# Optimization experiments

Hardware: AMD Instinct MI355X
Metric: run time of the kernel (lower is better)

The kernel has to match this reference:

```python
import jax, jax.numpy as jnp
import numpy as np

NEG_SLOPE = 0.2  # PyG GATConv default LeakyReLU slope


def add_self_loops(edge_index, n):
    loops = jnp.arange(n, dtype=edge_index.dtype)
    return jnp.concatenate([edge_index, jnp.stack([loops, loops])], axis=1)


def segment_softmax(e, seg, n):
    # e: [E, H], seg: [E] destination node ids
    m = jax.ops.segment_max(e, seg, num_segments=n)          # [N, H]
    ex = jnp.exp(e - m[seg])
    s = jax.ops.segment_sum(ex, seg, num_segments=n)          # [N, H]
    return ex / (s[seg] + 1e-16)


def gat_conv(x, edge_index, W, att_src, att_dst, bias, heads, concat):
    n = x.shape[0]
    c = W.shape[1] // heads
    ei = add_self_loops(edge_index, n)
    src, dst = ei[0], ei[1]
    h = (x @ W).reshape(n, heads, c)                          # [N, H, C]
    a_src = jnp.einsum('nhc,hc->nh', h, att_src)              # [N, H]
    a_dst = jnp.einsum('nhc,hc->nh', h, att_dst)
    e = a_src[src] + a_dst[dst]                               # [E, H]
    e = jax.nn.leaky_relu(e, NEG_SLOPE)
    alpha = segment_softmax(e, dst, n)                        # [E, H]
    msg = alpha[:, :, None] * h[src]                          # [E, H, C]
    out = jax.ops.segment_sum(msg, dst, num_segments=n)       # [N, H, C]
    if concat:
        out = out.reshape(n, heads * c)
    else:
        out = out.mean(axis=1)
    return out + bias


def setup_inputs() -> dict:
    key = jax.random.key(0)
    ks = jax.random.split(key, 16)
    N, E, IN, HID, H, OUT = 50000, 1600000, 512, 256, 8, 128
    s = 0.1
    return {
        'x': jax.random.normal(ks[0], (N, IN), jnp.float32),
        'edge_index': jax.random.randint(ks[1], (2, E), 0, N, jnp.int64),
        'edge_index_2': jax.random.randint(ks[2], (2, E), 0, N, jnp.int64),
        'W1': jax.random.normal(ks[3], (IN, HID * H), jnp.float32) * s,
        'att_src1': jax.random.normal(ks[4], (H, HID), jnp.float32) * s,
        'att_dst1': jax.random.normal(ks[5], (H, HID), jnp.float32) * s,
        'b1': jnp.zeros((HID * H,), jnp.float32),
        'W2': jax.random.normal(ks[6], (HID * H, OUT), jnp.float32) * s,
        'att_src2': jax.random.normal(ks[7], (1, OUT), jnp.float32) * s,
        'att_dst2': jax.random.normal(ks[8], (1, OUT), jnp.float32) * s,
        'b2': jnp.zeros((OUT,), jnp.float32),
        'W3': jax.random.normal(ks[9], (HID * H, OUT), jnp.float32) * s,
        'att_src3': jax.random.normal(ks[10], (1, OUT), jnp.float32) * s,
        'att_dst3': jax.random.normal(ks[11], (1, OUT), jnp.float32) * s,
        'b3': jnp.zeros((OUT,), jnp.float32),
    }


def reference(x, edge_index, edge_index_2, W1, att_src1, att_dst1, b1,
              W2, att_src2, att_dst2, b2, W3, att_src3, att_dst3, b3):
    # Inference mode: F.dropout and GATConv attention dropout are no-ops.
    emb = jax.nn.elu(gat_conv(x, edge_index, W1, att_src1, att_dst1, b1, heads=8, concat=True))
    x1 = gat_conv(emb, edge_index, W2, att_src2, att_dst2, b2, heads=1, concat=False)
    x2 = gat_conv(emb, edge_index_2, W3, att_src3, att_dst3, b3, heads=1, concat=False)
    logits = jax.nn.softmax(x1, axis=1)    # nn.Softmax() legacy dim -> 1 for 2D
    logits_2 = jax.nn.softmax(x2, axis=1)
    predictions = jnp.argmax(logits, axis=1)
    return (logits, logits_2, predictions)
```

## Files before the change

### kernel.cpp

```cpp
#include <hip/hip_runtime.h>
#include <hip/hip_bf16.h>
#include <math.h>

#define N_NODES 50000
#define E_EDGES 1600000
#define EP_EDGES (E_EDGES + N_NODES)
#define IN_F 512
#define HID 256
#define HEADS 8
#define OUTF 128

typedef unsigned short u16;
typedef __attribute__((ext_vector_type(8))) short short8;
typedef __attribute__((ext_vector_type(4))) float floatx4;

static __device__ __forceinline__ float eluf(float x) {
  return x > 0.f ? x : expm1f(x);
}

static __device__ __forceinline__ u16 bf16_hi(float v) {
  __hip_bfloat16 h = __float2bfloat16(v);
  return *(u16*)&h;
}
static __device__ __forceinline__ float bf16_f(u16 u) {
  __hip_bfloat16 h = *(__hip_bfloat16*)&u;
  return __bfloat162float(h);
}
static __device__ __forceinline__ void split3_bf16(float v, u16& h, u16& m, u16& l) {
  h = bf16_hi(v);
  float r1 = v - bf16_f(h);
  m = bf16_hi(r1);
  float r2 = r1 - bf16_f(m);
  l = bf16_hi(r2);
}

static __device__ __forceinline__ int clampi(int v, int n) {
  return v < 0 ? 0 : (v >= n ? n - 1 : v);
}


__global__ void k_detect(const int* __restrict__ ei, int* __restrict__ flag) {
  __shared__ int nz;
  if (threadIdx.x == 0) nz = 0;
  __syncthreads();
  for (int i = threadIdx.x; i < 4096; i += blockDim.x)
    if (ei[2 * i + 1] != 0) nz = 1;
  __syncthreads();
  if (threadIdx.x == 0) *flag = (nz ? 0 : 1);
}

__global__ void k_init_deg(int* __restrict__ deg, int n) {
  int i = blockIdx.x * 256 + threadIdx.x;
  if (i < n) deg[i] = 1;
}

__global__ void k_count(const int* __restrict__ ei, const int* __restrict__ flag,
                        int* __restrict__ deg, int E) {
  int e = blockIdx.x * 256 + threadIdx.x;
  if (e >= E) return;
  int f = *flag;
  int idx = E + e;
  int dst = clampi(ei[f ? 2 * idx : idx], N_NODES);
  atomicAdd(&deg[dst], 1);
}

__global__ __launch_bounds__(1024) void k_scan(const int* __restrict__ deg,
                                               int* __restrict__ rp, int n) {
  __shared__ int sw[16];
  __shared__ int s_run;
  int tid = threadIdx.x, lane = tid & 63, w = tid >> 6;
  if (tid == 0) s_run = 0;
  __syncthreads();
  for (int base = 0; base < n; base += 1024) {
    int i = base + tid;
    int v = (i < n) ? deg[i] : 0;
    int sv = v;
#pragma unroll
    for (int off = 1; off < 64; off <<= 1) {
      int t = __shfl_up(sv, off);
      if (lane >= off) sv += t;
    }
    if (lane == 63) sw[w] = sv;
    __syncthreads();
    if (w == 0) {
      int wsum = (lane < 16) ? sw[lane] : 0;
#pragma unroll
      for (int off = 1; off < 16; off <<= 1) {
        int t = __shfl_up(wsum, off);
        if (lane >= off) wsum += t;
      }
      if (lane < 16) sw[lane] = wsum;
    }
    __syncthreads();
    int woff = (w > 0) ? sw[w - 1] : 0;
    int run = s_run;
    if (i < n) rp[i + 1] = run + woff + sv;
    __syncthreads();
    if (tid == 1023) s_run = run + sw[15];
    __syncthreads();
  }
  if (tid == 0) rp[0] = 0;
}

__global__ void k_fill_self(const int* __restrict__ rp, int* __restrict__ wp,
                            int* __restrict__ col, int n) {
  int i = blockIdx.x * 256 + threadIdx.x;
  if (i < n) { int p = rp[i]; col[p] = i; wp[i] = p + 1; }
}

__global__ void k_fill_edges(const int* __restrict__ ei, const int* __restrict__ flag,
                             int* __restrict__ wp, int* __restrict__ col, int E) {
  int e = blockIdx.x * 256 + threadIdx.x;
  if (e >= E) return;
  int f = *flag;
  int src = clampi(ei[f ? 2 * e : e], N_NODES);
  int didx = E + e;
  int dst = clampi(ei[f ? 2 * didx : didx], N_NODES);
  int p = atomicAdd(&wp[dst], 1);
  col[p] = src;
}

__global__ void k_split3_t(const float* __restrict__ W, u16* __restrict__ H,
                           u16* __restrict__ Mv, u16* __restrict__ L,
                           int kshift, int kmask, int Nw, int total) {
  int idx = blockIdx.x * 256 + threadIdx.x;
  if (idx >= total) return;
  int n = idx >> kshift;
  int k = idx & kmask;
  u16 h, m, l;
  split3_bf16(W[(size_t)k * Nw + n], h, m, l);
  H[idx] = h;
  Mv[idx] = m;
  L[idx] = l;
}

__global__ __launch_bounds__(256) void k_watt1(
    const float* __restrict__ W1, const float* __restrict__ attS,
    const float* __restrict__ attD, float* __restrict__ watt) {
  int wid = (blockIdx.x * 256 + threadIdx.x) >> 6;
  int lane = threadIdx.x & 63;
  if (wid >= IN_F * HEADS) return;
  int k = wid >> 3, h = wid & 7;
  float4 wv = *(const float4*)&W1[(size_t)k * (HID * HEADS) + h * HID + lane * 4];
  float4 sv = *(const float4*)&attS[h * HID + lane * 4];
  float4 dv = *(const float4*)&attD[h * HID + lane * 4];
  float s = wv.x * sv.x + wv.y * sv.y + wv.z * sv.z + wv.w * sv.w;
  float d = wv.x * dv.x + wv.y * dv.y + wv.z * dv.z + wv.w * dv.w;
  for (int off = 32; off; off >>= 1) {
    s += __shfl_xor(s, off);
    d += __shfl_xor(d, off);
  }
  if (lane == 0) {
    watt[(size_t)(2 * h) * IN_F + k] = s;
    watt[(size_t)(2 * h + 1) * IN_F + k] = d;
  }
}

__global__ __launch_bounds__(256) void k_asad1(
    const float* __restrict__ x, const float* __restrict__ watt,
    float* __restrict__ asall, float* __restrict__ adall, int n) {
  int node = (blockIdx.x * 256 + threadIdx.x) >> 6;
  int lane = threadIdx.x & 63;
  if (node >= n) return;
  float4 x0 = *(const float4*)&x[(size_t)node * IN_F + lane * 8];
  float4 x1 = *(const float4*)&x[(size_t)node * IN_F + lane * 8 + 4];
  for (int h = 0; h < HEADS; ++h) {
    const float* ws = watt + (size_t)(2 * h) * IN_F + lane * 8;
    const float* wd = watt + (size_t)(2 * h + 1) * IN_F + lane * 8;
    float4 s0 = *(const float4*)ws, s1 = *(const float4*)(ws + 4);
    float4 d0 = *(const float4*)wd, d1 = *(const float4*)(wd + 4);
    float s = x0.x * s0.x + x0.y * s0.y + x0.z * s0.z + x0.w * s0.w
            + x1.x * s1.x + x1.y * s1.y + x1.z * s1.z + x1.w * s1.w;
    float d = x0.x * d0.x + x0.y * d0.y + x0.z * d0.z + x0.w * d0.w
            + x1.x * d1.x + x1.y * d1.y + x1.z * d1.z + x1.w * d1.w;
    for (int off = 32; off; off >>= 1) {
      s += __shfl_xor(s, off);
      d += __shfl_xor(d, off);
    }
    if (lane == 0) {
      asall[(size_t)h * n + node] = s;
      adall[(size_t)h * n + node] = d;
    }
  }
}

#define GBM 128
#define GBN 128
#define GBK 32
#define GM1 391

#define MFMA_BF16 __builtin_amdgcn_mfma_f32_16x16x32_bf16

__device__ __forceinline__ void gemm_epilogue(floatx4 acc[4][4], float* C,
                                              int ldc, int M, int accum,
                                              int row0, int col0, int wr,
                                              int wc, int lane) {
  int q = lane >> 4, n15 = lane & 15;
#pragma unroll
  for (int i = 0; i < 4; ++i) {
#pragma unroll
    for (int r = 0; r < 4; ++r) {
      int row = row0 + wr * 64 + i * 16 + q * 4 + r;
      if (row < M) {
#pragma unroll
        for (int j = 0; j < 4; ++j) {
          int cg = col0 + wc * 64 + j * 16 + n15;
          float v = acc[i][j][r];
          if (accum) v += C[(size_t)row * ldc + cg];
          C[(size_t)row * ldc + cg] = v;
        }
      }
    }
  }
}

__device__ __forceinline__ void gemm1_core(
    const float* __restrict__ X, int lda,
    const u16* __restrict__ Bh, const u16* __restrict__ Bm,
    const u16* __restrict__ Bl, int ldb,
    float* __restrict__ C, int ldc, int M, int K, int row0, int col0,
    u16* lds) {
  int tid = threadIdx.x;
  int lane = tid & 63, wave = tid >> 6;
  int wr = wave >> 1, wc = wave & 1;
  floatx4 acc[4][4] = {};
  int m0 = tid >> 2, m1 = (tid + 256) >> 2;
  int q0 = tid & 3;
  int lo0 = ((m0 >> 4) * 64 + q0 * 16 + (m0 & 15)) * 8;
  int lo1 = ((m1 >> 4) * 64 + q0 * 16 + (m1 & 15)) * 8;

  for (int k0 = 0; k0 < K; k0 += GBK) {
#pragma unroll
    for (int c = 0; c < 2; ++c) {
      int m = c ? m1 : m0;
      int lo = c ? lo1 : lo0;
      int gr = row0 + m;
      float f[8];
      if (gr < M) {
        float4 f0 = *(const float4*)(X + (size_t)gr * lda + k0 + q0 * 8);
        float4 f1 = *(const float4*)(X + (size_t)gr * lda + k0 + q0 * 8 + 4);
        f[0] = f0.x; f[1] = f0.y; f[2] = f0.z; f[3] = f0.w;
        f[4] = f1.x; f[5] = f1.y; f[6] = f1.z; f[7] = f1.w;
      } else {
#pragma unroll
        for (int e = 0; e < 8; ++e) f[e] = 0.f;
      }
      short8 vh, vm, vl;
#pragma unroll
      for (int e = 0; e < 8; ++e) {
        u16 h, m2, l;
        split3_bf16(f[e], h, m2, l);
        vh[e] = (short)h; vm[e] = (short)m2; vl[e] = (short)l;
      }
      *(short8*)&lds[lo] = vh;
      *(short8*)&lds[4096 + lo] = vm;
      *(short8*)&lds[8192 + lo] = vl;
    }
#pragma unroll
    for (int c = 0; c < 2; ++c) {
      int m = c ? m1 : m0;
      int lo = c ? lo1 : lo0;
      size_t go = (size_t)(col0 + m) * ldb + k0 + q0 * 8;
      *(short8*)&lds[12288 + lo] = *(const short8*)(Bh + go);
      *(short8*)&lds[16384 + lo] = *(const short8*)(Bm + go);
      *(short8*)&lds[20480 + lo] = *(const short8*)(Bl + go);
    }
    __syncthreads();
    short8 a_h[4], a_m[4], a_l[4];
#pragma unroll
    for (int i = 0; i < 4; ++i) {
      int o = ((wr * 4 + i) * 64 + lane) * 8;
      a_h[i] = *(short8*)&lds[o];
      a_m[i] = *(short8*)&lds[4096 + o];
      a_l[i] = *(short8*)&lds[8192 + o];
    }
#pragma unroll
    for (int j = 0; j < 4; ++j) {
      int o = ((wc * 4 + j) * 64 + lane) * 8;
      short8 b_h = *(short8*)&lds[12288 + o];
      short8 b_m = *(short8*)&lds[16384 + o];
      short8 b_l = *(short8*)&lds[20480 + o];
#pragma unroll
      for (int i = 0; i < 4; ++i) {
        acc[i][j] = MFMA_BF16(a_l[i], b_h, acc[i][j], 0, 0, 0);
        acc[i][j] = MFMA_BF16(a_m[i], b_m, acc[i][j], 0, 0, 0);
        acc[i][j] = MFMA_BF16(a_h[i], b_l, acc[i][j], 0, 0, 0);
        acc[i][j] = MFMA_BF16(a_m[i], b_h, acc[i][j], 0, 0, 0);
        acc[i][j] = MFMA_BF16(a_h[i], b_m, acc[i][j], 0, 0, 0);
        acc[i][j] = MFMA_BF16(a_h[i], b_h, acc[i][j], 0, 0, 0);
      }
    }
    __syncthreads();
  }
  gemm_epilogue(acc, C, ldc, M, 0, row0, col0, wr, wc, lane);
}

__global__ __launch_bounds__(256) void gemm1_k(
    const float* __restrict__ X, int lda,
    const u16* __restrict__ Bh, const u16* __restrict__ Bm,
    const u16* __restrict__ Bl, int ldb,
    float* __restrict__ C, int ldc, int M, int K) {
  __shared__ __align__(16) u16 lds[24576];
  gemm1_core(X, lda, Bh, Bm, Bl, ldb, C, ldc, M, K,
             blockIdx.x * GBM, blockIdx.y * GBN, lds);
}

__device__ __forceinline__ void gemm_core6(
    const u16* __restrict__ Ah, const u16* __restrict__ Am,
    const u16* __restrict__ Al, int lda,
    const u16* __restrict__ Bh, const u16* __restrict__ Bm,
    const u16* __restrict__ Bl, int ldb,
    float* __restrict__ C, int ldc, int M, int K, int row0, int col0,
    int accum, u16* lds) {
  int tid = threadIdx.x;
  int lane = tid & 63, wave = tid >> 6;
  int wr = wave >> 1, wc = wave & 1;
  floatx4 acc[4][4] = {};
  int m0 = tid >> 2, m1 = (tid + 256) >> 2;
  int q0 = tid & 3;
  int lo0 = ((m0 >> 4) * 64 + q0 * 16 + (m0 & 15)) * 8;
  int lo1 = ((m1 >> 4) * 64 + q0 * 16 + (m1 & 15)) * 8;
  for (int k0 = 0; k0 < K; k0 += GBK) {
#pragma unroll
    for (int c = 0; c < 2; ++c) {
      int m = c ? m1 : m0;
      int lo = c ? lo1 : lo0;
      int gr = row0 + m;
      short8 vh = {}, vm = {}, vl = {};
      if (gr < M) {
        size_t go = (size_t)gr * lda + k0 + q0 * 8;
        vh = *(const short8*)(Ah + go);
        vm = *(const short8*)(Am + go);
        vl = *(const short8*)(Al + go);
      }
      *(short8*)&lds[lo] = vh;
      *(short8*)&lds[4096 + lo] = vm;
      *(short8*)&lds[8192 + lo] = vl;
      size_t go = (size_t)(col0 + m) * ldb + k0 + q0 * 8;
      *(short8*)&lds[12288 + lo] = *(const short8*)(Bh + go);
      *(short8*)&lds[16384 + lo] = *(const short8*)(Bm + go);
      *(short8*)&lds[20480 + lo] = *(const short8*)(Bl + go);
    }
    __syncthreads();
    short8 a_h[4], a_m[4], a_l[4];
#pragma unroll
    for (int i = 0; i < 4; ++i) {
      int o = ((wr * 4 + i) * 64 + lane) * 8;
      a_h[i] = *(short8*)&lds[o];
      a_m[i] = *(short8*)&lds[4096 + o];
      a_l[i] = *(short8*)&lds[8192 + o];
    }
#pragma unroll
    for (int j = 0; j < 4; ++j) {
      int o = ((wc * 4 + j) * 64 + lane) * 8;
      short8 b_h = *(short8*)&lds[12288 + o];
      short8 b_m = *(short8*)&lds[16384 + o];
      short8 b_l = *(short8*)&lds[20480 + o];
#pragma unroll
      for (int i = 0; i < 4; ++i) {
        acc[i][j] = MFMA_BF16(a_l[i], b_h, acc[i][j], 0, 0, 0);
        acc[i][j] = MFMA_BF16(a_m[i], b_m, acc[i][j], 0, 0, 0);
        acc[i][j] = MFMA_BF16(a_h[i], b_l, acc[i][j], 0, 0, 0);
        acc[i][j] = MFMA_BF16(a_m[i], b_h, acc[i][j], 0, 0, 0);
        acc[i][j] = MFMA_BF16(a_h[i], b_m, acc[i][j], 0, 0, 0);
        acc[i][j] = MFMA_BF16(a_h[i], b_h, acc[i][j], 0, 0, 0);
      }
    }
    __syncthreads();
  }
  gemm_epilogue(acc, C, ldc, M, accum, row0, col0, wr, wc, lane);
}

__device__ __forceinline__ void gemm_core3(
    const u16* __restrict__ Ah, const u16* __restrict__ Am, int lda,
    const u16* __restrict__ Bh, const u16* __restrict__ Bm, int ldb,
    float* __restrict__ C, int ldc, int M, int K, int row0, int col0,
    int accum, u16* lds) {
  int tid = threadIdx.x;
  int lane = tid & 63, wave = tid >> 6;
  int wr = wave >> 1, wc = wave & 1;
  floatx4 acc[4][4] = {};
  int m0 = tid >> 2, m1 = (tid + 256) >> 2;
  int q0 = tid & 3;
  int lo0 = ((m0 >> 4) * 64 + q0 * 16 + (m0 & 15)) * 8;
  int lo1 = ((m1 >> 4) * 64 + q0 * 16 + (m1 & 15)) * 8;
  for (int k0 = 0; k0 < K; k0 += GBK) {
#pragma unroll
    for (int c = 0; c < 2; ++c) {
      int m = c ? m1 : m0;
      int lo = c ? lo1 : lo0;
      int gr = row0 + m;
      short8 vh = {}, vm = {};
      if (gr < M) {
        size_t go = (size_t)gr * lda + k0 + q0 * 8;
        vh = *(const short8*)(Ah + go);
        vm = *(const short8*)(Am + go);
      }
      *(short8*)&lds[lo] = vh;
      *(short8*)&lds[4096 + lo] = vm;
      size_t go = (size_t)(col0 + m) * ldb + k0 + q0 * 8;
      *(short8*)&lds[12288 + lo] = *(const short8*)(Bh + go);
      *(short8*)&lds[16384 + lo] = *(const short8*)(Bm + go);
    }
    __syncthreads();
    short8 a_h[4], a_m[4];
#pragma unroll
    for (int i = 0; i < 4; ++i) {
      int o = ((wr * 4 + i) * 64 + lane) * 8;
      a_h[i] = *(short8*)&lds[o];
      a_m[i] = *(short8*)&lds[4096 + o];
    }
#pragma unroll
    for (int j = 0; j < 4; ++j) {
      int o = ((wc * 4 + j) * 64 + lane) * 8;
      short8 b_h = *(short8*)&lds[12288 + o];
      short8 b_m = *(short8*)&lds[16384 + o];
#pragma unroll
      for (int i = 0; i < 4; ++i) {
        acc[i][j] = MFMA_BF16(a_m[i], b_h, acc[i][j], 0, 0, 0);
        acc[i][j] = MFMA_BF16(a_h[i], b_m, acc[i][j], 0, 0, 0);
        acc[i][j] = MFMA_BF16(a_h[i], b_h, acc[i][j], 0, 0, 0);
      }
    }
    __syncthreads();
  }
  gemm_epilogue(acc, C, ldc, M, accum, row0, col0, wr, wc, lane);
}

__global__ __launch_bounds__(256) void gemm23_k(
    const u16* __restrict__ Ah, const u16* __restrict__ Am,
    const u16* __restrict__ Al, int lda,
    const u16* __restrict__ B2h, const u16* __restrict__ B2m,
    const u16* __restrict__ B2l,
    const u16* __restrict__ B3h, const u16* __restrict__ B3m, int ldb,
    float* __restrict__ C2, float* __restrict__ C3, int ldc, int M, int K,
    int accum) {
  __shared__ __align__(16) u16 lds[24576];
  if (blockIdx.z == 0)
    gemm_core6(Ah, Am, Al, lda, B2h, B2m, B2l, ldb, C2, ldc, M, K,
               blockIdx.x * GBM, 0, accum, lds);
  else
    gemm_core3(Ah, Am, lda, B3h, B3m, ldb, C3, ldc, M, K,
               blockIdx.x * GBM, 0, accum, lds);
}

template <int C>
__global__ __launch_bounds__(256) void att_dot(
    const float* __restrict__ h, const float* __restrict__ attS,
    const float* __restrict__ attD, float* __restrict__ aS,
    float* __restrict__ aD, int n) {
  int node = (blockIdx.x * 256 + threadIdx.x) >> 6;
  int lane = threadIdx.x & 63;
  if (node >= n) return;
  float s = 0.f, d = 0.f;
  if (C == 256) {
    float4 hv = *(const float4*)&h[(size_t)node * C + lane * 4];
    float4 sv = *(const float4*)&attS[lane * 4];
    float4 dv = *(const float4*)&attD[lane * 4];
    s = hv.x * sv.x + hv.y * sv.y + hv.z * sv.z + hv.w * sv.w;
    d = hv.x * dv.x + hv.y * dv.y + hv.z * dv.z + hv.w * dv.w;
  } else {
    float2 hv = *(const float2*)&h[(size_t)node * C + lane * 2];
    float2 sv = *(const float2*)&attS[lane * 2];
    float2 dv = *(const float2*)&attD[lane * 2];
    s = hv.x * sv.x + hv.y * sv.y;
    d = hv.x * dv.x + hv.y * dv.y;
  }
  for (int off = 32; off; off >>= 1) {
    s += __shfl_xor(s, off);
    d += __shfl_xor(d, off);
  }
  if (lane == 0) { aS[node] = s; aD[node] = d; }
}

static __device__ __forceinline__ void aggr_l1_core(
    int node, int lane,
    const int* __restrict__ rp, const int* __restrict__ col,
    const float* __restrict__ aS, const float* __restrict__ aD,
    const float* __restrict__ h, const float* __restrict__ bias,
    u16* __restrict__ embH, u16* __restrict__ embM, u16* __restrict__ embL,
    int ecol0, int ldE, int n) {
  int s0 = rp[node], s1 = rp[node + 1];
  int d = s1 - s0;
  float ad = aD[node];
  float4 acc = make_float4(0.f, 0.f, 0.f, 0.f);

  if (d <= 64) {
    int c = 0;
    float e = -3.0e38f;
    if (lane < d) {
      c = clampi(col[s0 + lane], n);
      float t = aS[c] + ad;
      e = t >= 0.f ? t : 0.2f * t;
    }
    float m = e;
    for (int off = 32; off; off >>= 1) m = fmaxf(m, __shfl_xor(m, off));
    float ex = (lane < d) ? expf(e - m) : 0.f;
    float s = ex;
    for (int off = 32; off; off >>= 1) s += __shfl_xor(s, off);
    float al = ex * (1.f / (s + 1e-16f));
    int dd = d & ~15;
    for (int j = 0; j < dd; j += 16) {
#pragma unroll
      for (int t = 0; t < 16; ++t) {
        int ct = __shfl(c, j + t);
        float at = __shfl(al, j + t);
        float4 hv = *(const float4*)&h[(size_t)ct * HID + lane * 4];
        acc.x += at * hv.x; acc.y += at * hv.y;
        acc.z += at * hv.z; acc.w += at * hv.w;
      }
    }
    if (dd < d) {
#pragma unroll
      for (int t = 0; t < 16; ++t) {
        if (dd + t < d) {
          int ct = __shfl(c, dd + t);
          float at = __shfl(al, dd + t);
          float4 hv = *(const float4*)&h[(size_t)ct * HID + lane * 4];
          acc.x += at * hv.x; acc.y += at * hv.y;
          acc.z += at * hv.z; acc.w += at * hv.w;
        }
      }
    }
  } else {
    float m = -3.0e38f;
    for (int i = s0 + lane; i < s1; i += 64) {
      float e = aS[clampi(col[i], n)] + ad;
      e = e >= 0.f ? e : 0.2f * e;
      m = fmaxf(m, e);
    }
    for (int off = 32; off; off >>= 1) m = fmaxf(m, __shfl_xor(m, off));
    float sum = 0.f;
    for (int i = s0 + lane; i < s1; i += 64) {
      float e = aS[clampi(col[i], n)] + ad;
      e = e >= 0.f ? e : 0.2f * e;
      sum += expf(e - m);
    }
    for (int off = 32; off; off >>= 1) sum += __shfl_xor(sum, off);
    float inv = 1.f / (sum + 1e-16f);
    for (int i = s0; i < s1; ++i) {
      int ci = clampi(col[i], n);
      float e = aS[ci] + ad;
      e = e >= 0.f ? e : 0.2f * e;
      float a = expf(e - m) * inv;
      float4 hv = *(const float4*)&h[(size_t)ci * HID + lane * 4];
      acc.x += a * hv.x; acc.y += a * hv.y; acc.z += a * hv.z; acc.w += a * hv.w;
    }
  }

  float4 bb = *(const float4*)&bias[lane * 4];
  float v0 = eluf(acc.x + bb.x);
  float v1 = eluf(acc.y + bb.y);
  float v2 = eluf(acc.z + bb.z);
  float v3 = eluf(acc.w + bb.w);
  ushort4 uh, um, ul;
  split3_bf16(v0, uh.x, um.x, ul.x);
  split3_bf16(v1, uh.y, um.y, ul.y);
  split3_bf16(v2, uh.z, um.z, ul.z);
  split3_bf16(v3, uh.w, um.w, ul.w);
  size_t o = (size_t)node * ldE + ecol0 + lane * 4;
  *(ushort4*)&embH[o] = uh;
  *(ushort4*)&embM[o] = um;
  *(ushort4*)&embL[o] = ul;
}

__global__ __launch_bounds__(256) void aggr_l1_fused(
    const int* __restrict__ rp, const int* __restrict__ col,
    const float* __restrict__ aS, const float* __restrict__ aD,
    const float* __restrict__ h, const float* __restrict__ bias,
    u16* __restrict__ embH, u16* __restrict__ embM, u16* __restrict__ embL,
    int ecol0, int ldE, int n) {
  int node = (blockIdx.x * 256 + threadIdx.x) >> 6;
  int lane = threadIdx.x & 63;
  if (node >= n) return;
  aggr_l1_core(node, lane, rp, col, aS, aD, h, bias, embH, embM, embL,
               ecol0, ldE, n);
}

__global__ __launch_bounds__(256) void fused_step(
    const int* __restrict__ rp, const int* __restrict__ col,
    const float* __restrict__ aS, const float* __restrict__ aD,
    const float* __restrict__ hg, const float* __restrict__ bias,
    u16* __restrict__ embH, u16* __restrict__ embM, u16* __restrict__ embL,
    int ecol0, int ldE, int n,
    const float* __restrict__ X,
    const u16* __restrict__ B1h, const u16* __restrict__ B1m,
    const u16* __restrict__ B1l, float* __restrict__ h1out, int nG1,
    const u16* __restrict__ A23h, const u16* __restrict__ A23m,
    const u16* __restrict__ A23l,
    const u16* __restrict__ B2h, const u16* __restrict__ B2m,
    const u16* __restrict__ B2l,
    const u16* __restrict__ B3h, const u16* __restrict__ B3m,
    float* __restrict__ C2, float* __restrict__ C3, int accum, int nG23) {
  __shared__ __align__(16) u16 lds[24576];
  int nC = nG1 + nG23;
  int k = blockIdx.x;
  int q = k / 9, r = k - q * 9;
  if (r == 0 && q < nC) {
    if (q < nG1) {
      int bx = q % GM1, by = q / GM1;
      gemm1_core(X, IN_F, B1h, B1m, B1l, IN_F, h1out, HID, n, IN_F,
                 bx * GBM, by * GBN, lds);
    } else {
      int p = q - nG1;
      int z = p / GM1, bx = p - z * GM1;
      if (z == 0)
        gemm_core6(A23h, A23m, A23l, ldE, B2h, B2m, B2l, HID * HEADS,
                   C2, OUTF, n, HID, bx * GBM, 0, accum, lds);
      else
        gemm_core3(A23h, A23m, ldE, B3h, B3m, HID * HEADS,
                   C3, OUTF, n, HID, bx * GBM, 0, accum, lds);
    }
    return;
  }
  int skipped = q + (r ? 1 : 0);
  if (skipped > nC) skipped = nC;
  int aggrIdx = k - skipped;
  int node = aggrIdx * 4 + (threadIdx.x >> 6);
  int lane = threadIdx.x & 63;
  if (node >= n) return;
  aggr_l1_core(node, lane, rp, col, aS, aD, hg, bias, embH, embM, embL,
               ecol0, ldE, n);
}

__global__ __launch_bounds__(256) void aggr_l2_fused(
    const int* __restrict__ rp, const int* __restrict__ col,
    const float* __restrict__ aS, const float* __restrict__ aD,
    const float* __restrict__ h, const float* __restrict__ bias,
    float* __restrict__ out, float* __restrict__ pred, int n) {
  int node = (blockIdx.x * 256 + threadIdx.x) >> 6;
  int lane = threadIdx.x & 63;
  if (node >= n) return;
  int s0 = rp[node], s1 = rp[node + 1];
  int d = s1 - s0;
  float ad = aD[node];
  float2 acc = make_float2(0.f, 0.f);

  if (d <= 64) {
    int c = 0;
    float e = -3.0e38f;
    if (lane < d) {
      c = clampi(col[s0 + lane], n);
      float t = aS[c] + ad;
      e = t >= 0.f ? t : 0.2f * t;
    }
    float m = e;
    for (int off = 32; off; off >>= 1) m = fmaxf(m, __shfl_xor(m, off));
    float ex = (lane < d) ? expf(e - m) : 0.f;
    float s = ex;
    for (int off = 32; off; off >>= 1) s += __shfl_xor(s, off);
    float al = ex * (1.f / (s + 1e-16f));
    int dd = d & ~15;
    for (int j = 0; j < dd; j += 16) {
#pragma unroll
      for (int t = 0; t < 16; ++t) {
        int ct = __shfl(c, j + t);
        float at = __shfl(al, j + t);
        float2 hv = *(const float2*)&h[(size_t)ct * OUTF + lane * 2];
        acc.x += at * hv.x; acc.y += at * hv.y;
      }
    }
    if (dd < d) {
#pragma unroll
      for (int t = 0; t < 16; ++t) {
        if (dd + t < d) {
          int ct = __shfl(c, dd + t);
          float at = __shfl(al, dd + t);
          float2 hv = *(const float2*)&h[(size_t)ct * OUTF + lane * 2];
          acc.x += at * hv.x; acc.y += at * hv.y;
        }
      }
    }
  } else {
    float m = -3.0e38f;
    for (int i = s0 + lane; i < s1; i += 64) {
      float e = aS[clampi(col[i], n)] + ad;
      e = e >= 0.f ? e : 0.2f * e;
      m = fmaxf(m, e);
    }
    for (int off = 32; off; off >>= 1) m = fmaxf(m, __shfl_xor(m, off));
    float sum = 0.f;
    for (int i = s0 + lane; i < s1; i += 64) {
      float e = aS[clampi(col[i], n)] + ad;
      e = e >= 0.f ? e : 0.2f * e;
      sum += expf(e - m);
    }
    for (int off = 32; off; off >>= 1) sum += __shfl_xor(sum, off);
    float inv = 1.f / (sum + 1e-16f);
    for (int i = s0; i < s1; ++i) {
      int ci = clampi(col[i], n);
      float e = aS[ci] + ad;
      e = e >= 0.f ? e : 0.2f * e;
      float a = expf(e - m) * inv;
      float2 hv = *(const float2*)&h[(size_t)ci * OUTF + lane * 2];
      acc.x += a * hv.x; acc.y += a * hv.y;
    }
  }

  float2 bb = *(const float2*)&bias[lane * 2];
  acc.x += bb.x; acc.y += bb.y;

  float bv;
  int bi;
  if (acc.y > acc.x) { bv = acc.y; bi = 2 * lane + 1; }
  else               { bv = acc.x; bi = 2 * lane; }
  for (int off = 32; off; off >>= 1) {
    float ov = __shfl_xor(bv, off);
    int oi = __shfl_xor(bi, off);
    if (ov > bv || (ov == bv && oi < bi)) { bv = ov; bi = oi; }
  }
  float e0 = expf(acc.x - bv), e1 = expf(acc.y - bv);
  float ssum = e0 + e1;
  for (int off = 32; off; off >>= 1) ssum += __shfl_xor(ssum, off);
  float2 r;
  r.x = e0 / ssum;
  r.y = e1 / ssum;
  *(float2*)&out[(size_t)node * OUTF + lane * 2] = r;
  if (pred != nullptr && lane == 0) pred[node] = (float)bi;
}

extern "C" void kernel_launch(void* const* d_in, const int* in_sizes, int n_in,
                              void* d_out, int out_size, void* d_ws, size_t ws_size,
                              hipStream_t stream) {
  const int N = N_NODES, E = E_EDGES;
  const float* x     = (const float*)d_in[0];
  const int*   ei1   = (const int*)d_in[1];
  const int*   ei2   = (const int*)d_in[2];
  const float* W1    = (const float*)d_in[3];
  const float* attS1 = (const float*)d_in[4];
  const float* attD1 = (const float*)d_in[5];
  const float* b1    = (const float*)d_in[6];
  const float* W2    = (const float*)d_in[7];
  const float* attS2 = (const float*)d_in[8];
  const float* attD2 = (const float*)d_in[9];
  const float* b2    = (const float*)d_in[10];
  const float* W3    = (const float*)d_in[11];
  const float* attS3 = (const float*)d_in[12];
  const float* attD3 = (const float*)d_in[13];
  const float* b3    = (const float*)d_in[14];

  size_t needPipe =
      2 * ((size_t)EP_EDGES * 4) + 2 * ((size_t)(N + 1) * 4) +
      2 * ((size_t)N * 4) + 4096 +
      2 * ((size_t)N * HID * 4) +
      3 * ((size_t)N * 512 * 2) +
      (size_t)N * OUTF * 4 * 2 +
      3 * ((size_t)IN_F * HID * HEADS * 2) +
      6 * ((size_t)HID * HEADS * OUTF * 2) +
      2 * ((size_t)HEADS * N * 4) +
      4 * ((size_t)N * 4) +
      (size_t)2 * HEADS * IN_F * 4 +
      (size_t)(8 << 20);
  int pipe = (ws_size >= needPipe) ? 1 : 0;
  const int nbuf = pipe ? 2 : 1;
  const int ldE = pipe ? 512 : 256;

  char* ws = (char*)d_ws;
  size_t off = 0;
  auto take = [&](size_t bytes) {
    off = (off + 255) & ~(size_t)255;
    size_t o = off;
    off += bytes;
    return o;
  };
  int*   col1 = (int*)(ws + take((size_t)EP_EDGES * 4));
  int*   col2 = (int*)(ws + take((size_t)EP_EDGES * 4));
  int*   rp1  = (int*)(ws + take((size_t)(N + 1) * 4));
  int*   rp2  = (int*)(ws + take((size_t)(N + 1) * 4));
  int*   wp1  = (int*)(ws + take((size_t)N * 4));
  int*   wp2  = (int*)(ws + take((size_t)N * 4));
  int*   flag = (int*)(ws + take(256));
  float* h1hA = (float*)(ws + take((size_t)N * HID * 4 * nbuf));
  float* h1hB = pipe ? h1hA + (size_t)N * HID : h1hA;
  u16*   embH = (u16*)(ws + take((size_t)N * ldE * 2));
  u16*   embM = (u16*)(ws + take((size_t)N * ldE * 2));
  u16*   embL = (u16*)(ws + take((size_t)N * ldE * 2));
  float* h2   = (float*)(ws + take((size_t)N * OUTF * 4 * 2));
  float* h3   = h2 + (size_t)N * OUTF;
  u16*   W1Th = (u16*)(ws + take((size_t)IN_F * HID * HEADS * 2));
  u16*   W1Tm = (u16*)(ws + take((size_t)IN_F * HID * HEADS * 2));
  u16*   W1Tl = (u16*)(ws + take((size_t)IN_F * HID * HEADS * 2));
  u16*   W2Th = (u16*)(ws + take((size_t)HID * HEADS * OUTF * 2));
  u16*   W2Tm = (u16*)(ws + take((size_t)HID * HEADS * OUTF * 2));
  u16*   W2Tl = (u16*)(ws + take((size_t)HID * HEADS * OUTF * 2));
  u16*   W3Th = (u16*)(ws + take((size_t)HID * HEADS * OUTF * 2));
  u16*   W3Tm = (u16*)(ws + take((size_t)HID * HEADS * OUTF * 2));
  u16*   W3Tl = (u16*)(ws + take((size_t)HID * HEADS * OUTF * 2));
  float* asall = (float*)(ws + take((size_t)HEADS * N * 4));
  float* adall = (float*)(ws + take((size_t)HEADS * N * 4));
  float* as2  = (float*)(ws + take((size_t)N * 4));
  float* ad2  = (float*)(ws + take((size_t)N * 4));
  float* as3  = (float*)(ws + take((size_t)N * 4));
  float* ad3  = (float*)(ws + take((size_t)N * 4));
  float* watt = (float*)(ws + take((size_t)2 * HEADS * IN_F * 4));

  float* outp = (float*)d_out;
  float* x1   = outp;
  float* x2   = outp + (size_t)N * OUTF;
  float* pred = outp + (size_t)2 * N * OUTF;

  const int gN = (N + 255) / 256;
  const int gE = (E + 255) / 256;
  const int gW = (N + 3) / 4;

  k_split3_t<<<(IN_F * HID * HEADS + 255) / 256, 256, 0, stream>>>(
      W1, W1Th, W1Tm, W1Tl, 9, 511, HID * HEADS, IN_F * HID * HEADS);
  k_split3_t<<<(HID * HEADS * OUTF + 255) / 256, 256, 0, stream>>>(
      W2, W2Th, W2Tm, W2Tl, 11, 2047, OUTF, HID * HEADS * OUTF);
  k_split3_t<<<(HID * HEADS * OUTF + 255) / 256, 256, 0, stream>>>(
      W3, W3Th, W3Tm, W3Tl, 11, 2047, OUTF, HID * HEADS * OUTF);

  k_watt1<<<(IN_F * HEADS * 64 + 255) / 256, 256, 0, stream>>>(
      W1, attS1, attD1, watt);
  k_asad1<<<gW, 256, 0, stream>>>(x, watt, asall, adall, N);

  k_detect<<<1, 256, 0, stream>>>(ei1, flag);

  k_init_deg<<<gN, 256, 0, stream>>>(wp1, N);
  k_count<<<gE, 256, 0, stream>>>(ei1, flag, wp1, E);
  k_scan<<<1, 1024, 0, stream>>>(wp1, rp1, N);
  k_fill_self<<<gN, 256, 0, stream>>>(rp1, wp1, col1, N);
  k_fill_edges<<<gE, 256, 0, stream>>>(ei1, flag, wp1, col1, E);

  k_init_deg<<<gN, 256, 0, stream>>>(wp2, N);
  k_count<<<gE, 256, 0, stream>>>(ei2, flag, wp2, E);
  k_scan<<<1, 1024, 0, stream>>>(wp2, rp2, N);
  k_fill_self<<<gN, 256, 0, stream>>>(rp2, wp2, col2, N);
  k_fill_edges<<<gE, 256, 0, stream>>>(ei2, flag, wp2, col2, E);

  if (pipe) {
    float* buf[2] = {h1hA, h1hB};
    gemm1_k<<<dim3(GM1, 2), 256, 0, stream>>>(
        x, IN_F, W1Th, W1Tm, W1Tl, IN_F, buf[0], HID, N, IN_F);
    for (int h = 0; h < HEADS; ++h) {
      int nG1 = (h + 1 < HEADS) ? GM1 * 2 : 0;
      int nG23 = (h >= 1) ? GM1 * 2 : 0;
      int nC = nG1 + nG23;
      int T = gW + nC;
      if (9 * nC > T) T = 9 * nC;
      int hn = (h + 1 < HEADS) ? h + 1 : h;
      int hp = (h >= 1) ? h - 1 : 0;
      int sp = hp & 1;
      fused_step<<<T, 256, 0, stream>>>(
          rp1, col1, asall + (size_t)h * N, adall + (size_t)h * N,
          buf[h & 1], b1 + (size_t)h * HID,
          embH, embM, embL, (h & 1) * HID, ldE, N,
          x, W1Th + (size_t)hn * HID * IN_F, W1Tm + (size_t)hn * HID * IN_F,
          W1Tl + (size_t)hn * HID * IN_F, buf[(h + 1) & 1], nG1,
          embH + sp * HID, embM + sp * HID, embL + sp * HID,
          W2Th + (size_t)hp * HID, W2Tm + (size_t)hp * HID,
          W2Tl + (size_t)hp * HID,
          W3Th + (size_t)hp * HID, W3Tm + (size_t)hp * HID,
          h2, h3, hp > 0 ? 1 : 0, nG23);
    }
    gemm23_k<<<dim3(GM1, 1, 2), 256, 0, stream>>>(
        embH + HID, embM + HID, embL + HID, ldE,
        W2Th + (size_t)7 * HID, W2Tm + (size_t)7 * HID, W2Tl + (size_t)7 * HID,
        W3Th + (size_t)7 * HID, W3Tm + (size_t)7 * HID, HID * HEADS,
        h2, h3, OUTF, N, HID, 1);
  } else {
    for (int h = 0; h < HEADS; ++h) {
      gemm1_k<<<dim3(GM1, 2), 256, 0, stream>>>(
          x, IN_F,
          W1Th + (size_t)h * HID * IN_F, W1Tm + (size_t)h * HID * IN_F,
          W1Tl + (size_t)h * HID * IN_F, IN_F, h1hA, HID, N, IN_F);
      aggr_l1_fused<<<gW, 256, 0, stream>>>(
          rp1, col1, asall + (size_t)h * N, adall + (size_t)h * N, h1hA,
          b1 + (size_t)h * HID, embH, embM, embL, 0, ldE, N);
      gemm23_k<<<dim3(GM1, 1, 2), 256, 0, stream>>>(
          embH, embM, embL, ldE,
          W2Th + (size_t)h * HID, W2Tm + (size_t)h * HID,
          W2Tl + (size_t)h * HID,
          W3Th + (size_t)h * HID, W3Tm + (size_t)h * HID, HID * HEADS,
          h2, h3, OUTF, N, HID, h > 0 ? 1 : 0);
    }
  }

  att_dot<OUTF><<<gW, 256, 0, stream>>>(h2, attS2, attD2, as2, ad2, N);
  att_dot<OUTF><<<gW, 256, 0, stream>>>(h3, attS3, attD3, as3, ad3, N);
  aggr_l2_fused<<<gW, 256, 0, stream>>>(rp1, col1, as2, ad2, h2, b2, x1, pred, N);
  aggr_l2_fused<<<gW, 256, 0, stream>>>(rp2, col2, as3, ad3, h3, b3, x2, nullptr, N);
}
```

Measured before the change: 4.287 ms.

## Read low-part B tiles straight from global to shrink shared memory in fused step

Adds new GEMM cores for layer 1 and the 6-product layer-2 GEMM that stop staging the low bf16 part of B in shared memory. Each wave now loads that part directly from global memory, which lets the fused kernel's shared array shrink from 24576 to 20480 elements and may allow more resident blocks per CU. The aggregation inner loop is also unrolled by 8 instead of 16, lowering register pressure and shortening the tail. The cost is extra uncoalesced global loads of the B low part on every k-step.

```diff
diff --git a/kernel.cpp b/kernel.cpp
--- a/kernel.cpp
+++ b/kernel.cpp
@@ -417,6 +417,156 @@
       short8 b_m = *(short8*)&lds[16384 + o];
 #pragma unroll
       for (int i = 0; i < 4; ++i) {
+        acc[i][j] = MFMA_BF16(a_m[i], b_h, acc[i][j], 0, 0, 0);
+        acc[i][j] = MFMA_BF16(a_h[i], b_m, acc[i][j], 0, 0, 0);
+        acc[i][j] = MFMA_BF16(a_h[i], b_h, acc[i][j], 0, 0, 0);
+      }
+    }
+    __syncthreads();
+  }
+  gemm_epilogue(acc, C, ldc, M, accum, row0, col0, wr, wc, lane);
+}
+
+
+__device__ __forceinline__ void gemm1f_core(
+    const float* __restrict__ X, int lda,
+    const u16* __restrict__ Bh, const u16* __restrict__ Bm,
+    const u16* __restrict__ Bl, int ldb,
+    float* __restrict__ C, int ldc, int M, int K, int row0, int col0,
+    u16* lds) {
+  int tid = threadIdx.x;
+  int lane = tid & 63, wave = tid >> 6;
+  int wr = wave >> 1, wc = wave & 1;
+  floatx4 acc[4][4] = {};
+  int m0 = tid >> 2, m1 = (tid + 256) >> 2;
+  int q0 = tid & 3;
+  int lo0 = ((m0 >> 4) * 64 + q0 * 16 + (m0 & 15)) * 8;
+  int lo1 = ((m1 >> 4) * 64 + q0 * 16 + (m1 & 15)) * 8;
+  int bl_row = lane & 15, bl_k = (lane >> 4) * 8;
+
+  for (int k0 = 0; k0 < K; k0 += GBK) {
+#pragma unroll
+    for (int c = 0; c < 2; ++c) {
+      int m = c ? m1 : m0;
+      int lo = c ? lo1 : lo0;
+      int gr = row0 + m;
+      float f[8];
+      if (gr < M) {
+        float4 f0 = *(const float4*)(X + (size_t)gr * lda + k0 + q0 * 8);
+        float4 f1 = *(const float4*)(X + (size_t)gr * lda + k0 + q0 * 8 + 4);
+        f[0] = f0.x; f[1] = f0.y; f[2] = f0.z; f[3] = f0.w;
+        f[4] = f1.x; f[5] = f1.y; f[6] = f1.z; f[7] = f1.w;
+      } else {
+#pragma unroll
+        for (int e = 0; e < 8; ++e) f[e] = 0.f;
+      }
+      short8 vh, vm, vl;
+#pragma unroll
+      for (int e = 0; e < 8; ++e) {
+        u16 h, m2, l;
+        split3_bf16(f[e], h, m2, l);
+        vh[e] = (short)h; vm[e] = (short)m2; vl[e] = (short)l;
+      }
+      *(short8*)&lds[lo] = vh;
+      *(short8*)&lds[4096 + lo] = vm;
+      *(short8*)&lds[8192 + lo] = vl;
+    }
+#pragma unroll
+    for (int c = 0; c < 2; ++c) {
+      int m = c ? m1 : m0;
+      int lo = c ? lo1 : lo0;
+      size_t go = (size_t)(col0 + m) * ldb + k0 + q0 * 8;
+      *(short8*)&lds[12288 + lo] = *(const short8*)(Bh + go);
+      *(short8*)&lds[16384 + lo] = *(const short8*)(Bm + go);
+    }
+    __syncthreads();
+    short8 a_h[4], a_m[4], a_l[4];
+#pragma unroll
+    for (int i = 0; i < 4; ++i) {
+      int o = ((wr * 4 + i) * 64 + lane) * 8;
+      a_h[i] = *(short8*)&lds[o];
+      a_m[i] = *(short8*)&lds[4096 + o];
+      a_l[i] = *(short8*)&lds[8192 + o];
+    }
+#pragma unroll
+    for (int j = 0; j < 4; ++j) {
+      int o = ((wc * 4 + j) * 64 + lane) * 8;
+      short8 b_h = *(short8*)&lds[12288 + o];
+      short8 b_m = *(short8*)&lds[16384 + o];
+      short8 b_l = *(const short8*)(Bl +
+          (size_t)(col0 + (wc * 4 + j) * 16 + bl_row) * ldb + k0 + bl_k);
+#pragma unroll
+      for (int i = 0; i < 4; ++i) {
+        acc[i][j] = MFMA_BF16(a_l[i], b_h, acc[i][j], 0, 0, 0);
+        acc[i][j] = MFMA_BF16(a_m[i], b_m, acc[i][j], 0, 0, 0);
+        acc[i][j] = MFMA_BF16(a_h[i], b_l, acc[i][j], 0, 0, 0);
+        acc[i][j] = MFMA_BF16(a_m[i], b_h, acc[i][j], 0, 0, 0);
+        acc[i][j] = MFMA_BF16(a_h[i], b_m, acc[i][j], 0, 0, 0);
+        acc[i][j] = MFMA_BF16(a_h[i], b_h, acc[i][j], 0, 0, 0);
+      }
+    }
+    __syncthreads();
+  }
+  gemm_epilogue(acc, C, ldc, M, 0, row0, col0, wr, wc, lane);
+}
+
+__device__ __forceinline__ void gemm6f_core(
+    const u16* __restrict__ Ah, const u16* __restrict__ Am,
+    const u16* __restrict__ Al, int lda,
+    const u16* __restrict__ Bh, const u16* __restrict__ Bm,
+    const u16* __restrict__ Bl, int ldb,
+    float* __restrict__ C, int ldc, int M, int K, int row0, int col0,
+    int accum, u16* lds) {
+  int tid = threadIdx.x;
+  int lane = tid & 63, wave = tid >> 6;
+  int wr = wave >> 1, wc = wave & 1;
+  floatx4 acc[4][4] = {};
+  int m0 = tid >> 2, m1 = (tid + 256) >> 2;
+  int q0 = tid & 3;
+  int lo0 = ((m0 >> 4) * 64 + q0 * 16 + (m0 & 15)) * 8;
+  int lo1 = ((m1 >> 4) * 64 + q0 * 16 + (m1 & 15)) * 8;
+  int bl_row = lane & 15, bl_k = (lane >> 4) * 8;
+  for (int k0 = 0; k0 < K; k0 += GBK) {
+#pragma unroll
+    for (int c = 0; c < 2; ++c) {
+      int m = c ? m1 : m0;
+      int lo = c ? lo1 : lo0;
+      int gr = row0 + m;
+      short8 vh = {}, vm = {}, vl = {};
+      if (gr < M) {
+        size_t go = (size_t)gr * lda + k0 + q0 * 8;
+        vh = *(const short8*)(Ah + go);
+        vm = *(const short8*)(Am + go);
+        vl = *(const short8*)(Al + go);
+      }
+      *(short8*)&lds[lo] = vh;
+      *(short8*)&lds[4096 + lo] = vm;
+      *(short8*)&lds[8192 + lo] = vl;
+      size_t go = (size_t)(col0 + m) * ldb + k0 + q0 * 8;
+      *(short8*)&lds[12288 + lo] = *(const short8*)(Bh + go);
+      *(short8*)&lds[16384 + lo] = *(const short8*)(Bm + go);
+    }
+    __syncthreads();
+    short8 a_h[4], a_m[4], a_l[4];
+#pragma unroll
+    for (int i = 0; i < 4; ++i) {
+      int o = ((wr * 4 + i) * 64 + lane) * 8;
+      a_h[i] = *(short8*)&lds[o];
+      a_m[i] = *(short8*)&lds[4096 + o];
+      a_l[i] = *(short8*)&lds[8192 + o];
+    }
+#pragma unroll
+    for (int j = 0; j < 4; ++j) {
+      int o = ((wc * 4 + j) * 64 + lane) * 8;
+      short8 b_h = *(short8*)&lds[12288 + o];
+      short8 b_m = *(short8*)&lds[16384 + o];
+      short8 b_l = *(const short8*)(Bl +
+          (size_t)(col0 + (wc * 4 + j) * 16 + bl_row) * ldb + k0 + bl_k);
+#pragma unroll
+      for (int i = 0; i < 4; ++i) {
+        acc[i][j] = MFMA_BF16(a_l[i], b_h, acc[i][j], 0, 0, 0);
+        acc[i][j] = MFMA_BF16(a_m[i], b_m, acc[i][j], 0, 0, 0);
+        acc[i][j] = MFMA_BF16(a_h[i], b_l, acc[i][j], 0, 0, 0);
         acc[i][j] = MFMA_BF16(a_m[i], b_h, acc[i][j], 0, 0, 0);
         acc[i][j] = MFMA_BF16(a_h[i], b_m, acc[i][j], 0, 0, 0);
         acc[i][j] = MFMA_BF16(a_h[i], b_h, acc[i][j], 0, 0, 0);
@@ -499,10 +649,10 @@
     float s = ex;
     for (int off = 32; off; off >>= 1) s += __shfl_xor(s, off);
     float al = ex * (1.f / (s + 1e-16f));
-    int dd = d & ~15;
-    for (int j = 0; j < dd; j += 16) {
-#pragma unroll
-      for (int t = 0; t < 16; ++t) {
+    int d8 = d & ~7;
+    for (int j = 0; j < d8; j += 8) {
+#pragma unroll
+      for (int t = 0; t < 8; ++t) {
         int ct = __shfl(c, j + t);
         float at = __shfl(al, j + t);
         float4 hv = *(const float4*)&h[(size_t)ct * HID + lane * 4];
@@ -510,12 +660,12 @@
         acc.z += at * hv.z; acc.w += at * hv.w;
       }
     }
-    if (dd < d) {
-#pragma unroll
-      for (int t = 0; t < 16; ++t) {
-        if (dd + t < d) {
-          int ct = __shfl(c, dd + t);
-          float at = __shfl(al, dd + t);
+    if (d8 < d) {
+#pragma unroll
+      for (int t = 0; t < 8; ++t) {
+        if (d8 + t < d) {
+          int ct = __shfl(c, d8 + t);
+          float at = __shfl(al, d8 + t);
           float4 hv = *(const float4*)&h[(size_t)ct * HID + lane * 4];
           acc.x += at * hv.x; acc.y += at * hv.y;
           acc.z += at * hv.z; acc.w += at * hv.w;
@@ -592,21 +742,21 @@
     const u16* __restrict__ B2l,
     const u16* __restrict__ B3h, const u16* __restrict__ B3m,
     float* __restrict__ C2, float* __restrict__ C3, int accum, int nG23) {
-  __shared__ __align__(16) u16 lds[24576];
+  __shared__ __align__(16) u16 lds[20480];
   int nC = nG1 + nG23;
   int k = blockIdx.x;
   int q = k / 9, r = k - q * 9;
   if (r == 0 && q < nC) {
     if (q < nG1) {
       int bx = q % GM1, by = q / GM1;
-      gemm1_core(X, IN_F, B1h, B1m, B1l, IN_F, h1out, HID, n, IN_F,
-                 bx * GBM, by * GBN, lds);
+      gemm1f_core(X, IN_F, B1h, B1m, B1l, IN_F, h1out, HID, n, IN_F,
+                  bx * GBM, by * GBN, lds);
     } else {
       int p = q - nG1;
       int z = p / GM1, bx = p - z * GM1;
       if (z == 0)
-        gemm_core6(A23h, A23m, A23l, ldE, B2h, B2m, B2l, HID * HEADS,
-                   C2, OUTF, n, HID, bx * GBM, 0, accum, lds);
+        gemm6f_core(A23h, A23m, A23l, ldE, B2h, B2m, B2l, HID * HEADS,
+                    C2, OUTF, n, HID, bx * GBM, 0, accum, lds);
       else
         gemm_core3(A23h, A23m, ldE, B3h, B3m, HID * HEADS,
                    C3, OUTF, n, HID, bx * GBM, 0, accum, lds);
```

New measurement: 4.047 ms. -5.6%, faster.

## Overlap second-graph CSR build with layer-1 GEMMs and merge tail kernels

Applied to the files above, without the earlier changes.

Builds the CSR for the second edge set alongside compute: degree counting rides in a prologue kernel with the first GEMM, and edge filling is appended to the first fused_step launch. The paired att_dot and aggr_l2 launches for the two output branches are each merged into one dual-grid launch. The unroll depth of the layer-1 aggregation gather also drops from 16 to 8. This is meant to hide the serial CSR-build kernels and cut launch count and tail under-utilisation. The cost is extra branching, and edge order within col2 now comes from atomics running concurrently with other work.

```diff
diff --git a/kernel.cpp b/kernel.cpp
--- a/kernel.cpp
+++ b/kernel.cpp
@@ -305,6 +305,28 @@
              blockIdx.x * GBM, blockIdx.y * GBN, lds);
 }
 
+__global__ __launch_bounds__(256) void prologue_k(
+    const float* __restrict__ X,
+    const u16* __restrict__ Bh, const u16* __restrict__ Bm,
+    const u16* __restrict__ Bl, float* __restrict__ C, int M,
+    const int* __restrict__ ei2, const int* __restrict__ flag,
+    int* __restrict__ deg2, int E2, int nG) {
+  __shared__ __align__(16) u16 lds[24576];
+  int b = blockIdx.x;
+  if (b < nG) {
+    int bx = b % GM1, by = b / GM1;
+    gemm1_core(X, IN_F, Bh, Bm, Bl, IN_F, C, HID, M, IN_F,
+               bx * GBM, by * GBN, lds);
+    return;
+  }
+  int e = (b - nG) * 256 + threadIdx.x;
+  if (e >= E2) return;
+  int f = *flag;
+  int idx = E2 + e;
+  int dst = clampi(ei2[f ? 2 * idx : idx], N_NODES);
+  atomicAdd(&deg2[dst], 1);
+}
+
 __device__ __forceinline__ void gemm_core6(
     const u16* __restrict__ Ah, const u16* __restrict__ Am,
     const u16* __restrict__ Al, int lda,
@@ -444,33 +466,33 @@
                blockIdx.x * GBM, 0, accum, lds);
 }
 
-template <int C>
-__global__ __launch_bounds__(256) void att_dot(
-    const float* __restrict__ h, const float* __restrict__ attS,
-    const float* __restrict__ attD, float* __restrict__ aS,
-    float* __restrict__ aD, int n) {
-  int node = (blockIdx.x * 256 + threadIdx.x) >> 6;
+__global__ __launch_bounds__(256) void att_dot_dual(
+    const float* __restrict__ h2, const float* __restrict__ h3,
+    const float* __restrict__ s2, const float* __restrict__ d2,
+    const float* __restrict__ s3, const float* __restrict__ d3,
+    float* __restrict__ as2, float* __restrict__ ad2,
+    float* __restrict__ as3, float* __restrict__ ad3, int n, int gW) {
+  int b = blockIdx.x;
+  int second = (b >= gW) ? 1 : 0;
+  int bb = second ? b - gW : b;
+  const float* h  = second ? h3 : h2;
+  const float* sS = second ? s3 : s2;
+  const float* sD = second ? d3 : d2;
+  float* oS = second ? as3 : as2;
+  float* oD = second ? ad3 : ad2;
+  int node = (bb * 256 + threadIdx.x) >> 6;
   int lane = threadIdx.x & 63;
   if (node >= n) return;
-  float s = 0.f, d = 0.f;
-  if (C == 256) {
-    float4 hv = *(const float4*)&h[(size_t)node * C + lane * 4];
-    float4 sv = *(const float4*)&attS[lane * 4];
-    float4 dv = *(const float4*)&attD[lane * 4];
-    s = hv.x * sv.x + hv.y * sv.y + hv.z * sv.z + hv.w * sv.w;
-    d = hv.x * dv.x + hv.y * dv.y + hv.z * dv.z + hv.w * dv.w;
-  } else {
-    float2 hv = *(const float2*)&h[(size_t)node * C + lane * 2];
-    float2 sv = *(const float2*)&attS[lane * 2];
-    float2 dv = *(const float2*)&attD[lane * 2];
-    s = hv.x * sv.x + hv.y * sv.y;
-    d = hv.x * dv.x + hv.y * dv.y;
-  }
+  float2 hv = *(const float2*)&h[(size_t)node * OUTF + lane * 2];
+  float2 sv = *(const float2*)&sS[lane * 2];
+  float2 dv = *(const float2*)&sD[lane * 2];
+  float s = hv.x * sv.x + hv.y * sv.y;
+  float d = hv.x * dv.x + hv.y * dv.y;
   for (int off = 32; off; off >>= 1) {
     s += __shfl_xor(s, off);
     d += __shfl_xor(d, off);
   }
-  if (lane == 0) { aS[node] = s; aD[node] = d; }
+  if (lane == 0) { oS[node] = s; oD[node] = d; }
 }
 
 static __device__ __forceinline__ void aggr_l1_core(
@@ -499,10 +521,10 @@
     float s = ex;
     for (int off = 32; off; off >>= 1) s += __shfl_xor(s, off);
     float al = ex * (1.f / (s + 1e-16f));
-    int dd = d & ~15;
-    for (int j = 0; j < dd; j += 16) {
-#pragma unroll
-      for (int t = 0; t < 16; ++t) {
+    int d8 = d & ~7;
+    for (int j = 0; j < d8; j += 8) {
+#pragma unroll
+      for (int t = 0; t < 8; ++t) {
         int ct = __shfl(c, j + t);
         float at = __shfl(al, j + t);
         float4 hv = *(const float4*)&h[(size_t)ct * HID + lane * 4];
@@ -510,12 +532,12 @@
         acc.z += at * hv.z; acc.w += at * hv.w;
       }
     }
-    if (dd < d) {
-#pragma unroll
-      for (int t = 0; t < 16; ++t) {
-        if (dd + t < d) {
-          int ct = __shfl(c, dd + t);
-          float at = __shfl(al, dd + t);
+    if (d8 < d) {
+#pragma unroll
+      for (int t = 0; t < 8; ++t) {
+        if (d8 + t < d) {
+          int ct = __shfl(c, d8 + t);
+          float at = __shfl(al, d8 + t);
           float4 hv = *(const float4*)&h[(size_t)ct * HID + lane * 4];
           acc.x += at * hv.x; acc.y += at * hv.y;
           acc.z += at * hv.z; acc.w += at * hv.w;
@@ -591,7 +613,9 @@
     const u16* __restrict__ B2h, const u16* __restrict__ B2m,
     const u16* __restrict__ B2l,
     const u16* __restrict__ B3h, const u16* __restrict__ B3m,
-    float* __restrict__ C2, float* __restrict__ C3, int accum, int nG23) {
+    float* __restrict__ C2, float* __restrict__ C3, int accum, int nG23,
+    const int* __restrict__ ei2, const int* __restrict__ flag,
+    int* __restrict__ wp2, int* __restrict__ col2, int nE, int E2) {
   __shared__ __align__(16) u16 lds[24576];
   int nC = nG1 + nG23;
   int k = blockIdx.x;
@@ -616,19 +640,47 @@
   int skipped = q + (r ? 1 : 0);
   if (skipped > nC) skipped = nC;
   int aggrIdx = k - skipped;
-  int node = aggrIdx * 4 + (threadIdx.x >> 6);
-  int lane = threadIdx.x & 63;
-  if (node >= n) return;
-  aggr_l1_core(node, lane, rp, col, aS, aD, hg, bias, embH, embM, embL,
-               ecol0, ldE, n);
-}
-
-__global__ __launch_bounds__(256) void aggr_l2_fused(
-    const int* __restrict__ rp, const int* __restrict__ col,
-    const float* __restrict__ aS, const float* __restrict__ aD,
-    const float* __restrict__ h, const float* __restrict__ bias,
-    float* __restrict__ out, float* __restrict__ pred, int n) {
-  int node = (blockIdx.x * 256 + threadIdx.x) >> 6;
+  int nb = (n + 3) >> 2;
+  if (aggrIdx < nb) {
+    int node = aggrIdx * 4 + (threadIdx.x >> 6);
+    int lane = threadIdx.x & 63;
+    if (node >= n) return;
+    aggr_l1_core(node, lane, rp, col, aS, aD, hg, bias, embH, embM, embL,
+                 ecol0, ldE, n);
+    return;
+  }
+  int e = (aggrIdx - nb) * 256 + (int)threadIdx.x;
+  if (e >= E2) return;
+  int f = *flag;
+  int src = clampi(ei2[f ? 2 * e : e], N_NODES);
+  int didx = E2 + e;
+  int dst = clampi(ei2[f ? 2 * didx : didx], N_NODES);
+  int p = atomicAdd(&wp2[dst], 1);
+  col2[p] = src;
+}
+
+__global__ __launch_bounds__(256) void aggr_l2_dual(
+    const int* __restrict__ rp1, const int* __restrict__ col1,
+    const float* __restrict__ as2, const float* __restrict__ ad2,
+    const float* __restrict__ h2, const float* __restrict__ b2,
+    float* __restrict__ x1, float* __restrict__ pred,
+    const int* __restrict__ rp2, const int* __restrict__ col2,
+    const float* __restrict__ as3, const float* __restrict__ ad3,
+    const float* __restrict__ h3, const float* __restrict__ b3,
+    float* __restrict__ x2, int n, int gW) {
+  int b = blockIdx.x;
+  int second = (b >= gW) ? 1 : 0;
+  int bb = second ? b - gW : b;
+  const int* rp = second ? rp2 : rp1;
+  const int* col = second ? col2 : col1;
+  const float* aS = second ? as3 : as2;
+  const float* aD = second ? ad3 : ad2;
+  const float* h = second ? h3 : h2;
+  const float* bias = second ? b3 : b2;
+  float* out = second ? x2 : x1;
+  float* pr = second ? nullptr : pred;
+
+  int node = (bb * 256 + threadIdx.x) >> 6;
   int lane = threadIdx.x & 63;
   if (node >= n) return;
   int s0 = rp[node], s1 = rp[node + 1];
@@ -697,8 +749,8 @@
     }
   }
 
-  float2 bb = *(const float2*)&bias[lane * 2];
-  acc.x += bb.x; acc.y += bb.y;
+  float2 bb2 = *(const float2*)&bias[lane * 2];
+  acc.x += bb2.x; acc.y += bb2.y;
 
   float bv;
   int bi;
@@ -716,7 +768,7 @@
   r.x = e0 / ssum;
   r.y = e1 / ssum;
   *(float2*)&out[(size_t)node * OUTF + lane * 2] = r;
-  if (pred != nullptr && lane == 0) pred[node] = (float)bi;
+  if (pr != nullptr && lane == 0) pr[node] = (float)bi;
 }
 
 extern "C" void kernel_launch(void* const* d_in, const int* in_sizes, int n_in,
@@ -822,21 +874,20 @@
   k_fill_self<<<gN, 256, 0, stream>>>(rp1, wp1, col1, N);
   k_fill_edges<<<gE, 256, 0, stream>>>(ei1, flag, wp1, col1, E);
 
-  k_init_deg<<<gN, 256, 0, stream>>>(wp2, N);
-  k_count<<<gE, 256, 0, stream>>>(ei2, flag, wp2, E);
-  k_scan<<<1, 1024, 0, stream>>>(wp2, rp2, N);
-  k_fill_self<<<gN, 256, 0, stream>>>(rp2, wp2, col2, N);
-  k_fill_edges<<<gE, 256, 0, stream>>>(ei2, flag, wp2, col2, E);
-
   if (pipe) {
     float* buf[2] = {h1hA, h1hB};
-    gemm1_k<<<dim3(GM1, 2), 256, 0, stream>>>(
-        x, IN_F, W1Th, W1Tm, W1Tl, IN_F, buf[0], HID, N, IN_F);
+    k_init_deg<<<gN, 256, 0, stream>>>(wp2, N);
+    prologue_k<<<GM1 * 2 + gE, 256, 0, stream>>>(
+        x, W1Th, W1Tm, W1Tl, buf[0], N, ei2, flag, wp2, E, GM1 * 2);
+    k_scan<<<1, 1024, 0, stream>>>(wp2, rp2, N);
+    k_fill_self<<<gN, 256, 0, stream>>>(rp2, wp2, col2, N);
+
     for (int h = 0; h < HEADS; ++h) {
       int nG1 = (h + 1 < HEADS) ? GM1 * 2 : 0;
       int nG23 = (h >= 1) ? GM1 * 2 : 0;
       int nC = nG1 + nG23;
-      int T = gW + nC;
+      int nE = (h == 0) ? gE : 0;
+      int T = gW + nE + nC;
       if (9 * nC > T) T = 9 * nC;
       int hn = (h + 1 < HEADS) ? h + 1 : h;
       int hp = (h >= 1) ? h - 1 : 0;
@@ -851,7 +902,8 @@
           W2Th + (size_t)hp * HID, W2Tm + (size_t)hp * HID,
           W2Tl + (size_t)hp * HID,
           W3Th + (size_t)hp * HID, W3Tm + (size_t)hp * HID,
-          h2, h3, hp > 0 ? 1 : 0, nG23);
+          h2, h3, hp > 0 ? 1 : 0, nG23,
+          ei2, flag, wp2, col2, nE, E);
     }
     gemm23_k<<<dim3(GM1, 1, 2), 256, 0, stream>>>(
         embH + HID, embM + HID, embL + HID, ldE,
@@ -859,6 +911,11 @@
         W3Th + (size_t)7 * HID, W3Tm + (size_t)7 * HID, HID * HEADS,
         h2, h3, OUTF, N, HID, 1);
   } else {
+    k_init_deg<<<gN, 256, 0, stream>>>(wp2, N);
+    k_count<<<gE, 256, 0, stream>>>(ei2, flag, wp2, E);
+    k_scan<<<1, 1024, 0, stream>>>(wp2, rp2, N);
+    k_fill_self<<<gN, 256, 0, stream>>>(rp2, wp2, col2, N);
+    k_fill_edges<<<gE, 256, 0, stream>>>(ei2, flag, wp2, col2, E);
     for (int h = 0; h < HEADS; ++h) {
       gemm1_k<<<dim3(GM1, 2), 256, 0, stream>>>(
           x, IN_F,
@@ -876,8 +933,9 @@
     }
   }
 
-  att_dot<OUTF><<<gW, 256, 0, stream>>>(h2, attS2, attD2, as2, ad2, N);
-  att_dot<OUTF><<<gW, 256, 0, stream>>>(h3, attS3, attD3, as3, ad3, N);
-  aggr_l2_fused<<<gW, 256, 0, stream>>>(rp1, col1, as2, ad2, h2, b2, x1, pred, N);
-  aggr_l2_fused<<<gW, 256, 0, stream>>>(rp2, col2, as3, ad3, h3, b3, x2, nullptr, N);
-}
+  att_dot_dual<<<2 * gW, 256, 0, stream>>>(
+      h2, h3, attS2, attD2, attS3, attD3, as2, ad2, as3, ad3, N, gW);
+  aggr_l2_dual<<<2 * gW, 256, 0, stream>>>(
+      rp1, col1, as2, ad2, h2, b2, x1, pred,
+      rp2, col2, as3, ad3, h3, b3, x2, N, gW);
+}
```

Result: faster. 3.977 ms (-7.2%).
